# Kernel optimization log

Measured on AMD Instinct MI355X. Metric: run time of the kernel, lower is better.

## Reference

```python
import jax, jax.numpy as jnp
import numpy as np

N_NODES = 100000


def _gcn_conv(h, src, dst, norm, W, b):
    # h: [N, F_in] -> [N, F_out]; aggregate normalized messages over edges
    h = h @ W                                   # transform first (cheaper messages)
    msg = h[src] * norm[:, None]                # [E_tot, F_out]
    agg = jax.ops.segment_sum(msg, dst, num_segments=N_NODES)
    return agg + b


def setup_inputs() -> dict:
    key = jax.random.key(0)
    k1, k2, k3, k4 = jax.random.split(key, 4)
    x = jax.random.normal(k1, (N_NODES, 256), dtype=jnp.float32)
    edge_index = jax.random.randint(k2, (2, 1600000), 0, N_NODES, dtype=jnp.int64)
    W1 = jax.random.normal(k3, (256, 128), dtype=jnp.float32) * (1.0 / np.sqrt(256))
    b1 = jnp.zeros((128,), dtype=jnp.float32)
    W2 = jax.random.normal(k4, (128, 40), dtype=jnp.float32) * (1.0 / np.sqrt(128))
    b2 = jnp.zeros((40,), dtype=jnp.float32)
    return {"x": x, "edge_index": edge_index, "W1": W1, "b1": b1, "W2": W2, "b2": b2}


def reference(x, edge_index, W1, b1, W2, b2):
    # add self-loops
    loop = jnp.arange(N_NODES, dtype=edge_index.dtype)
    src = jnp.concatenate([edge_index[0], loop])
    dst = jnp.concatenate([edge_index[1], loop])
    # symmetric normalization D^{-1/2} (A+I) D^{-1/2}
    deg = jax.ops.segment_sum(jnp.ones_like(dst, dtype=x.dtype), dst, num_segments=N_NODES)
    dinv = jax.lax.rsqrt(jnp.maximum(deg, 1.0))
    norm = dinv[src] * dinv[dst]                # [E_tot]

    h = _gcn_conv(x, src, dst, norm, W1, b1)
    h = jax.nn.relu(h)                          # dropout p=0 / eval -> identity
    h = _gcn_conv(h, src, dst, norm, W2, b2)
    return jax.nn.log_softmax(h, axis=1)
```

## Files before the change

### kernel.cpp

```cpp
#include <hip/hip_runtime.h>
#include <hip/hip_fp8.h>
#include <math.h>

#define N_NODES 100000
#define N_EDGES 1600000
#define F_IN 256
#define F_H 128
#define F_OUT 40

#define BIN_SHIFT 9
#define BIN_NODES 512
#define NBIN 196
#define CAP 12288
#define CNT_PAD 16
#define PART_CHUNK 8192

typedef __attribute__((ext_vector_type(8))) short bf16x8;
typedef __attribute__((ext_vector_type(4))) float floatx4;
typedef __attribute__((ext_vector_type(2))) float floatx2;
typedef __attribute__((ext_vector_type(2))) unsigned int uintx2;

__device__ __forceinline__ unsigned short f2bf(float f) {
    unsigned int u = __float_as_uint(f);
    u += 0x7fffu + ((u >> 16) & 1u);
    return (unsigned short)(u >> 16);
}
__device__ __forceinline__ float bf2f(unsigned short s) { return __uint_as_float(((unsigned int)s) << 16); }

#if defined(__has_builtin)
#if __has_builtin(__builtin_amdgcn_cvt_pk_fp8_f32)
#define HAVE_PK_ENC 1
#endif
#if __has_builtin(__builtin_amdgcn_cvt_pk_f32_fp8)
#define HAVE_PK_DEC 1
#endif
#if __has_builtin(__builtin_amdgcn_cvt_f32_fp8)
#define HAVE_SC_DEC 1
#endif
#endif

__device__ __forceinline__ unsigned char f2f8(float f) {
#ifdef HAVE_PK_ENC
    int r = __builtin_amdgcn_cvt_pk_fp8_f32(f, f, 0, false);
    return (unsigned char)(r & 0xff);
#else
    __hip_fp8_e4m3 t(f);
    return (unsigned char)t.__x;
#endif
}
__device__ __forceinline__ float f82f(unsigned char b) {
#ifdef HAVE_SC_DEC
    return __builtin_amdgcn_cvt_f32_fp8((int)b, 0);
#else
    __hip_fp8_e4m3 t; t.__x = (__hip_fp8_storage_t)b;
    return (float)t;
#endif
}
__device__ __forceinline__ floatx2 f8x2tof(unsigned short u) {
#ifdef HAVE_PK_DEC
    return __builtin_amdgcn_cvt_pk_f32_fp8((int)u, false);
#else
    floatx2 r;
    r.x = f82f((unsigned char)(u & 0xff));
    r.y = f82f((unsigned char)(u >> 8));
    return r;
#endif
}

__global__ void k_zero(int* p, int n) {
    int i = blockIdx.x * blockDim.x + threadIdx.x;
    if (i < n) p[i] = 0;
}

__global__ __launch_bounds__(256) void k_part(const int* __restrict__ eidx,
                                              int* __restrict__ gcnt,
                                              unsigned int* __restrict__ parts) {
    __shared__ int hist[4][NBIN];
    __shared__ int sbase[NBIN];
    __shared__ int rcnt[NBIN];
    const int tid = threadIdx.x;
    const int wv = tid >> 6;
    for (int i = tid; i < NBIN; i += 256) {
        hist[0][i] = 0; hist[1][i] = 0; hist[2][i] = 0; hist[3][i] = 0; rcnt[i] = 0;
    }
    __syncthreads();
    const int e0 = blockIdx.x * PART_CHUNK;
    const int e1 = min(e0 + PART_CHUNK, N_EDGES);
    for (int e = e0 + tid; e < e1; e += 256) {
        int d = eidx[N_EDGES + e];
        atomicAdd(&hist[wv][d >> BIN_SHIFT], 1);
    }
    __syncthreads();
    for (int b = tid; b < NBIN; b += 256) {
        int tot = hist[0][b] + hist[1][b] + hist[2][b] + hist[3][b];
        int old = atomicAdd(&gcnt[b * CNT_PAD], tot);
        sbase[b] = b * CAP + old;
    }
    __syncthreads();
    for (int e = e0 + tid; e < e1; e += 256) {
        int d = eidx[N_EDGES + e];
        int s = eidx[e];
        int b = d >> BIN_SHIFT;
        int r = atomicAdd(&rcnt[b], 1);
        parts[sbase[b] + r] = ((unsigned int)s << BIN_SHIFT) | (unsigned int)(d & (BIN_NODES - 1));
    }
}

__global__ __launch_bounds__(256) void k_build(const unsigned int* __restrict__ parts,
                                               const int* __restrict__ gcnt,
                                               int* __restrict__ rowptr,
                                               float* __restrict__ dinv,
                                               int* __restrict__ csr_src) {
    __shared__ int deg[4][BIN_NODES];
    __shared__ int cur[BIN_NODES];
    __shared__ int scan[256];
    const int tid = threadIdx.x;
    const int wv = tid >> 6;
    const int g = blockIdx.x;

    scan[tid] = (tid < NBIN) ? gcnt[tid * CNT_PAD] : 0;
    __syncthreads();
    for (int off = 1; off < 256; off <<= 1) {
        int v = 0;
        if (tid >= off) v = scan[tid - off];
        __syncthreads();
        if (tid >= off) scan[tid] += v;
        __syncthreads();
    }
    const int binBase = (g == 0) ? 0 : scan[g - 1];
    const int cntg = scan[g] - binBase;

    for (int i = tid; i < BIN_NODES; i += 256) {
        deg[0][i] = 0; deg[1][i] = 0; deg[2][i] = 0; deg[3][i] = 0;
    }
    __syncthreads();

    const unsigned int* pp = parts + (size_t)g * CAP;
    for (int i = tid; i < cntg; i += 256)
        atomicAdd(&deg[wv][pp[i] & (BIN_NODES - 1)], 1);
    __syncthreads();

    const int n0 = 2 * tid, n1 = 2 * tid + 1;
    const int d0 = deg[0][n0] + deg[1][n0] + deg[2][n0] + deg[3][n0];
    const int d1 = deg[0][n1] + deg[1][n1] + deg[2][n1] + deg[3][n1];
    scan[tid] = d0 + d1;
    __syncthreads();
    for (int off = 1; off < 256; off <<= 1) {
        int v = 0;
        if (tid >= off) v = scan[tid - off];
        __syncthreads();
        if (tid >= off) scan[tid] += v;
        __syncthreads();
    }
    const int pre = (tid == 0) ? 0 : scan[tid - 1];
    const int p0 = binBase + pre;
    const int p1 = p0 + d0;
    const int node0 = g * BIN_NODES + n0;
    if (node0 < N_NODES)     { rowptr[node0]     = p0; dinv[node0]     = rsqrtf((float)d0 + 1.0f); }
    if (node0 + 1 < N_NODES) { rowptr[node0 + 1] = p1; dinv[node0 + 1] = rsqrtf((float)d1 + 1.0f); }
    cur[n0] = p0;
    cur[n1] = p1;
    __syncthreads();

    for (int i = tid; i < cntg; i += 256) {
        unsigned int u = pp[i];
        int pos = atomicAdd(&cur[u & (BIN_NODES - 1)], 1);
        csr_src[pos] = (int)(u >> BIN_SHIFT);
    }
    if (g == NBIN - 1 && tid == 0) rowptr[N_NODES] = N_EDGES;
}

__global__ void k_cvt_w(const float* __restrict__ W1, const float* __restrict__ W2,
                        short* __restrict__ W1t, short* __restrict__ W2t) {
    int b = blockIdx.x, t = threadIdx.x;
    if (b < 128) {
        int idx = b * 256 + t;
        int n = idx >> 8, k = idx & 255;
        W1t[n * 256 + k] = (short)f2bf(W1[k * 128 + n]);
    } else {
        int idx = (b - 128) * 256 + t;
        if (idx < 48 * 128) {
            int n = idx >> 7, k = idx & 127;
            float v = (n < F_OUT) ? W2[k * F_OUT + n] : 0.f;
            W2t[n * 128 + k] = (short)f2bf(v);
        }
    }
}

__global__ __launch_bounds__(256) void k_gemm1_mfma(const float* __restrict__ x,
                                                    const short* __restrict__ W1t,
                                                    const float* __restrict__ dinv,
                                                    unsigned char* __restrict__ h1f8) {
    __shared__ short As[64 * 40];
    __shared__ short Bs[128 * 40];
    __shared__ float Ds[64];
    const int tid = threadIdx.x;
    const int row0 = blockIdx.x * 64;
    const int w = tid >> 6, l = tid & 63;
    const int l15 = l & 15, q = l >> 4;
    const int ar = tid >> 2;
    const int ak = (tid & 3) * 8;
    const int bn = tid >> 1;
    const int bk = (tid & 1) * 16;

    if (tid < 64) {
        int r = row0 + tid;
        Ds[tid] = (r < N_NODES) ? dinv[r] : 0.f;
    }

    floatx4 acc[4][2];
#pragma unroll
    for (int mt = 0; mt < 4; ++mt)
#pragma unroll
        for (int nt = 0; nt < 2; ++nt) acc[mt][nt] = (floatx4)0.f;

    const bool arow_ok = (row0 + ar) < N_NODES;
    const float* xp = x + (size_t)(row0 + ar) * F_IN;

    for (int k0 = 0; k0 < F_IN; k0 += 32) {
        bf16x8 av;
        if (arow_ok) {
            float4 f0 = *(const float4*)(xp + k0 + ak);
            float4 f1 = *(const float4*)(xp + k0 + ak + 4);
            av[0] = (short)f2bf(f0.x); av[1] = (short)f2bf(f0.y);
            av[2] = (short)f2bf(f0.z); av[3] = (short)f2bf(f0.w);
            av[4] = (short)f2bf(f1.x); av[5] = (short)f2bf(f1.y);
            av[6] = (short)f2bf(f1.z); av[7] = (short)f2bf(f1.w);
        } else {
            av = (bf16x8)0;
        }
        *(bf16x8*)&As[ar * 40 + ak] = av;
        *(bf16x8*)&Bs[bn * 40 + bk]     = *(const bf16x8*)&W1t[bn * 256 + k0 + bk];
        *(bf16x8*)&Bs[bn * 40 + bk + 8] = *(const bf16x8*)&W1t[bn * 256 + k0 + bk + 8];
        __syncthreads();

        bf16x8 af[4], bfr[2];
#pragma unroll
        for (int mt = 0; mt < 4; ++mt)
            af[mt] = *(const bf16x8*)&As[(mt * 16 + l15) * 40 + q * 8];
#pragma unroll
        for (int nt = 0; nt < 2; ++nt)
            bfr[nt] = *(const bf16x8*)&Bs[(w * 32 + nt * 16 + l15) * 40 + q * 8];
#pragma unroll
        for (int mt = 0; mt < 4; ++mt)
#pragma unroll
            for (int nt = 0; nt < 2; ++nt)
                acc[mt][nt] = __builtin_amdgcn_mfma_f32_16x16x32_bf16(af[mt], bfr[nt], acc[mt][nt], 0, 0, 0);
        __syncthreads();
    }
#pragma unroll
    for (int mt = 0; mt < 4; ++mt) {
#pragma unroll
        for (int nt = 0; nt < 2; ++nt) {
            int col = w * 32 + nt * 16 + l15;
#pragma unroll
            for (int r = 0; r < 4; ++r) {
                int rl = mt * 16 + q * 4 + r;
                int row = row0 + rl;
                if (row < N_NODES)
                    h1f8[(size_t)row * F_H + col] = f2f8(acc[mt][nt][r] * Ds[rl]);
            }
        }
    }
}

__global__ __launch_bounds__(256) void k_spmm1(const int* __restrict__ rowptr,
                                               const int* __restrict__ csr_src,
                                               const unsigned int* __restrict__ h1d,
                                               const float* __restrict__ dinv,
                                               const float* __restrict__ b1,
                                               uintx2* __restrict__ agg1p2) {
    const int half = threadIdx.x >> 5;
    const int p = threadIdx.x & 31;
    int node = blockIdx.x * 8 + half;
    bool valid = node < N_NODES;
    int nd = valid ? node : 0;
    int beg = rowptr[nd];
    int end = valid ? rowptr[nd + 1] : beg;
    float dv = dinv[nd];

    unsigned int su = h1d[(size_t)nd * 32 + p];
    floatx2 s01 = f8x2tof((unsigned short)(su & 0xffffu));
    floatx2 s23 = f8x2tof((unsigned short)(su >> 16));
    float A0 = s01.x, A1 = s01.y, A2 = s23.x, A3 = s23.y;
    float B0 = 0.f, B1 = 0.f, B2 = 0.f, B3 = 0.f;
    float C0 = 0.f, C1 = 0.f, C2 = 0.f, C3 = 0.f;
    float D0 = 0.f, D1 = 0.f, D2 = 0.f, D3 = 0.f;

    int i = beg;
    for (; i + 3 < end; i += 4) {
        int s0 = csr_src[i], s1 = csr_src[i + 1], s2 = csr_src[i + 2], s3 = csr_src[i + 3];
        unsigned int u0 = h1d[(size_t)s0 * 32 + p];
        unsigned int u1 = h1d[(size_t)s1 * 32 + p];
        unsigned int u2 = h1d[(size_t)s2 * 32 + p];
        unsigned int u3 = h1d[(size_t)s3 * 32 + p];
        floatx2 a01 = f8x2tof((unsigned short)(u0 & 0xffffu));
        floatx2 a23 = f8x2tof((unsigned short)(u0 >> 16));
        floatx2 b01 = f8x2tof((unsigned short)(u1 & 0xffffu));
        floatx2 b23 = f8x2tof((unsigned short)(u1 >> 16));
        floatx2 c01 = f8x2tof((unsigned short)(u2 & 0xffffu));
        floatx2 c23 = f8x2tof((unsigned short)(u2 >> 16));
        floatx2 d01 = f8x2tof((unsigned short)(u3 & 0xffffu));
        floatx2 d23 = f8x2tof((unsigned short)(u3 >> 16));
        A0 += a01.x; A1 += a01.y; A2 += a23.x; A3 += a23.y;
        B0 += b01.x; B1 += b01.y; B2 += b23.x; B3 += b23.y;
        C0 += c01.x; C1 += c01.y; C2 += c23.x; C3 += c23.y;
        D0 += d01.x; D1 += d01.y; D2 += d23.x; D3 += d23.y;
    }
    for (; i < end; ++i) {
        unsigned int u0 = h1d[(size_t)csr_src[i] * 32 + p];
        floatx2 a01 = f8x2tof((unsigned short)(u0 & 0xffffu));
        floatx2 a23 = f8x2tof((unsigned short)(u0 >> 16));
        A0 += a01.x; A1 += a01.y; A2 += a23.x; A3 += a23.y;
    }

    float4 bb = *(const float4*)&b1[4 * p];
    float v0 = fmaf((A0 + B0) + (C0 + D0), dv, bb.x);
    float v1 = fmaf((A1 + B1) + (C1 + D1), dv, bb.y);
    float v2 = fmaf((A2 + B2) + (C2 + D2), dv, bb.z);
    float v3 = fmaf((A3 + B3) + (C3 + D3), dv, bb.w);
    v0 = v0 > 0.f ? v0 : 0.f;
    v1 = v1 > 0.f ? v1 : 0.f;
    v2 = v2 > 0.f ? v2 : 0.f;
    v3 = v3 > 0.f ? v3 : 0.f;
    if (valid) {
        uintx2 o;
        o.x = ((unsigned int)f2bf(v1) << 16) | f2bf(v0);
        o.y = ((unsigned int)f2bf(v3) << 16) | f2bf(v2);
        agg1p2[(size_t)node * 32 + p] = o;
    }
}

__global__ __launch_bounds__(256) void k_gemm2_mfma(const unsigned short* __restrict__ agg1b,
                                                    const short* __restrict__ W2t,
                                                    const float* __restrict__ dinv,
                                                    unsigned char* __restrict__ h2f8) {
    __shared__ short As[128 * 40];
    __shared__ short Bs[48 * 136];
    __shared__ float Ds[128];
    const int tid = threadIdx.x;
    const int row0 = blockIdx.x * 128;
    const int w = tid >> 6, l = tid & 63;
    const int l15 = l & 15, q = l >> 4;
    const int ar = tid >> 1;
    const int ak = (tid & 1) * 16;

#pragma unroll
    for (int i = 0; i < 3; ++i) {
        int c = tid * 3 + i;
        int n = c >> 4, koff = (c & 15) * 8;
        *(bf16x8*)&Bs[n * 136 + koff] = *(const bf16x8*)&W2t[n * 128 + koff];
    }
    if (tid < 128) {
        int r = row0 + tid;
        Ds[tid] = (r < N_NODES) ? dinv[r] : 0.f;
    }

    floatx4 acc[2][3];
#pragma unroll
    for (int a = 0; a < 2; ++a)
#pragma unroll
        for (int nt = 0; nt < 3; ++nt) acc[a][nt] = (floatx4)0.f;

    const bool arow_ok = (row0 + ar) < N_NODES;
    const unsigned short* ap = agg1b + (size_t)(row0 + ar) * F_H;

    for (int k0 = 0; k0 < F_H; k0 += 32) {
        bf16x8 a0, a1;
        if (arow_ok) {
            a0 = *(const bf16x8*)(ap + k0 + ak);
            a1 = *(const bf16x8*)(ap + k0 + ak + 8);
        } else {
            a0 = (bf16x8)0; a1 = (bf16x8)0;
        }
        *(bf16x8*)&As[ar * 40 + ak]     = a0;
        *(bf16x8*)&As[ar * 40 + ak + 8] = a1;
        __syncthreads();

        bf16x8 af[2], bfr[3];
#pragma unroll
        for (int a = 0; a < 2; ++a)
            af[a] = *(const bf16x8*)&As[((w * 2 + a) * 16 + l15) * 40 + q * 8];
#pragma unroll
        for (int nt = 0; nt < 3; ++nt)
            bfr[nt] = *(const bf16x8*)&Bs[(nt * 16 + l15) * 136 + k0 + q * 8];
#pragma unroll
        for (int a = 0; a < 2; ++a)
#pragma unroll
            for (int nt = 0; nt < 3; ++nt)
                acc[a][nt] = __builtin_amdgcn_mfma_f32_16x16x32_bf16(af[a], bfr[nt], acc[a][nt], 0, 0, 0);
        __syncthreads();
    }
#pragma unroll
    for (int a = 0; a < 2; ++a) {
#pragma unroll
        for (int nt = 0; nt < 3; ++nt) {
            int col = nt * 16 + l15;
#pragma unroll
            for (int r = 0; r < 4; ++r) {
                int rl = (w * 2 + a) * 16 + q * 4 + r;
                int row = row0 + rl;
                if (row < N_NODES && col < F_OUT)
                    h2f8[(size_t)row * F_OUT + col] = f2f8(acc[a][nt][r] * Ds[rl]);
            }
        }
    }
}

__global__ __launch_bounds__(256) void k_spmm2_lsm(const int* __restrict__ rowptr,
                                                   const int* __restrict__ csr_src,
                                                   const unsigned int* __restrict__ h2d,
                                                   const float* __restrict__ dinv,
                                                   const float* __restrict__ b2,
                                                   float* __restrict__ out) {
    const int qid = threadIdx.x >> 4;
    const int p = threadIdx.x & 15;
    int node = blockIdx.x * 16 + qid;
    bool nvalid = node < N_NODES;
    bool valid = nvalid && (p < 10);
    int nd = nvalid ? node : 0;
    int beg = 0, end = 0;
    if (valid) { beg = rowptr[nd]; end = rowptr[nd + 1]; }
    float dv = dinv[nd];

    float A0 = 0.f, A1 = 0.f, A2 = 0.f, A3 = 0.f;
    float B0 = 0.f, B1 = 0.f, B2 = 0.f, B3 = 0.f;
    if (valid) {
        unsigned int su = h2d[(size_t)nd * 10 + p];
        floatx2 t0 = f8x2tof((unsigned short)(su & 0xffffu));
        floatx2 t1 = f8x2tof((unsigned short)(su >> 16));
        A0 = t0.x; A1 = t0.y; A2 = t1.x; A3 = t1.y;
    }
    int i = beg;
    for (; i + 1 < end; i += 2) {
        int s0 = csr_src[i], s1 = csr_src[i + 1];
        unsigned int u0 = h2d[(size_t)s0 * 10 + p];
        unsigned int u1 = h2d[(size_t)s1 * 10 + p];
        floatx2 a01 = f8x2tof((unsigned short)(u0 & 0xffffu));
        floatx2 a23 = f8x2tof((unsigned short)(u0 >> 16));
        floatx2 b01 = f8x2tof((unsigned short)(u1 & 0xffffu));
        floatx2 b23 = f8x2tof((unsigned short)(u1 >> 16));
        A0 += a01.x; A1 += a01.y; A2 += a23.x; A3 += a23.y;
        B0 += b01.x; B1 += b01.y; B2 += b23.x; B3 += b23.y;
    }
    if (i < end) {
        unsigned int u0 = h2d[(size_t)csr_src[i] * 10 + p];
        floatx2 a01 = f8x2tof((unsigned short)(u0 & 0xffffu));
        floatx2 a23 = f8x2tof((unsigned short)(u0 >> 16));
        A0 += a01.x; A1 += a01.y; A2 += a23.x; A3 += a23.y;
    }

    float v0 = -INFINITY, v1 = -INFINITY, v2 = -INFINITY, v3 = -INFINITY;
    if (valid) {
        float4 bb = *(const float4*)&b2[4 * p];
        v0 = fmaf(A0 + B0, dv, bb.x);
        v1 = fmaf(A1 + B1, dv, bb.y);
        v2 = fmaf(A2 + B2, dv, bb.z);
        v3 = fmaf(A3 + B3, dv, bb.w);
    }
    float m = fmaxf(fmaxf(v0, v1), fmaxf(v2, v3));
#pragma unroll
    for (int off = 1; off < 16; off <<= 1) m = fmaxf(m, __shfl_xor(m, off, 16));
    float e = 0.f;
    if (valid) e = expf(v0 - m) + expf(v1 - m) + expf(v2 - m) + expf(v3 - m);
#pragma unroll
    for (int off = 1; off < 16; off <<= 1) e += __shfl_xor(e, off, 16);
    if (valid) {
        float ls = logf(e);
        float4 o;
        o.x = v0 - m - ls; o.y = v1 - m - ls; o.z = v2 - m - ls; o.w = v3 - m - ls;
        *(float4*)&out[(size_t)node * F_OUT + 4 * p] = o;
    }
}

extern "C" void kernel_launch(void* const* d_in, const int* in_sizes, int n_in,
                              void* d_out, int out_size, void* d_ws, size_t ws_size,
                              hipStream_t stream) {
    const float* x = (const float*)d_in[0];
    const int* eidx = (const int*)d_in[1];
    const float* W1 = (const float*)d_in[2];
    const float* b1 = (const float*)d_in[3];
    const float* W2 = (const float*)d_in[4];
    const float* b2 = (const float*)d_in[5];
    float* out = (float*)d_out;

    char* ws = (char*)d_ws;
    int*   gcnt      = (int*)  (ws);
    int*   rowptr    = (int*)  (ws + 400512);
    int*   csr_src   = (int*)  (ws + 1200528);
    float* dinv      = (float*)(ws + 7600528);
    short* W1t       = (short*)(ws + 8000528);
    short* W2t       = (short*)(ws + 8066064);
    unsigned char*  h1f8  = (unsigned char*) (ws + 8078352);
    unsigned short* agg1b = (unsigned short*)(ws + 20878352);
    unsigned int*   parts = (unsigned int*)  (ws + 20878352);
    unsigned char*  h2f8  = (unsigned char*) (ws + 46478352);

    k_zero<<<(NBIN * CNT_PAD + 255) / 256, 256, 0, stream>>>(gcnt, NBIN * CNT_PAD);
    k_part<<<(N_EDGES + PART_CHUNK - 1) / PART_CHUNK, 256, 0, stream>>>(eidx, gcnt, parts);
    k_build<<<NBIN, 256, 0, stream>>>(parts, gcnt, rowptr, dinv, csr_src);

    k_cvt_w<<<152, 256, 0, stream>>>(W1, W2, W1t, W2t);

    k_gemm1_mfma<<<(N_NODES + 63) / 64, 256, 0, stream>>>(x, W1t, dinv, h1f8);
    k_spmm1<<<(N_NODES + 7) / 8, 256, 0, stream>>>(rowptr, csr_src,
                                                   (const unsigned int*)h1f8, dinv, b1,
                                                   (uintx2*)agg1b);
    k_gemm2_mfma<<<(N_NODES + 127) / 128, 256, 0, stream>>>(agg1b, W2t, dinv, h2f8);
    k_spmm2_lsm<<<(N_NODES + 15) / 16, 256, 0, stream>>>(rowptr, csr_src,
                                                         (const unsigned int*)h2f8, dinv, b2, out);
}
```

Baseline: 340.3 us.

## Split hidden features into four column planes for cache-friendly SpMM gathers

GEMM1 now keeps W1 fragments in registers with no LDS staging, and writes h1 as four 32-column fp8 planes instead of one row-major 128-column array. SpMM1 runs once per plane, so the random gathers for each pass hit a 3.2 MB table that fits in cache better, at the cost of reading the CSR indices four times and launching four kernels. Nontemporal loads and stores are added for streamed x, csr indices and outputs to reduce cache pollution.

```diff
diff --git a/kernel.cpp b/kernel.cpp
--- a/kernel.cpp
+++ b/kernel.cpp
@@ -190,96 +190,70 @@
 __global__ __launch_bounds__(256) void k_gemm1_mfma(const float* __restrict__ x,
                                                     const short* __restrict__ W1t,
                                                     const float* __restrict__ dinv,
-                                                    unsigned char* __restrict__ h1f8) {
-    __shared__ short As[64 * 40];
-    __shared__ short Bs[128 * 40];
-    __shared__ float Ds[64];
+                                                    unsigned char* __restrict__ h1q) {
     const int tid = threadIdx.x;
-    const int row0 = blockIdx.x * 64;
     const int w = tid >> 6, l = tid & 63;
     const int l15 = l & 15, q = l >> 4;
-    const int ar = tid >> 2;
-    const int ak = (tid & 3) * 8;
-    const int bn = tid >> 1;
-    const int bk = (tid & 1) * 16;
-
-    if (tid < 64) {
-        int r = row0 + tid;
-        Ds[tid] = (r < N_NODES) ? dinv[r] : 0.f;
-    }
-
-    floatx4 acc[4][2];
-#pragma unroll
-    for (int mt = 0; mt < 4; ++mt)
-#pragma unroll
-        for (int nt = 0; nt < 2; ++nt) acc[mt][nt] = (floatx4)0.f;
-
-    const bool arow_ok = (row0 + ar) < N_NODES;
-    const float* xp = x + (size_t)(row0 + ar) * F_IN;
-
-    for (int k0 = 0; k0 < F_IN; k0 += 32) {
-        bf16x8 av;
-        if (arow_ok) {
-            float4 f0 = *(const float4*)(xp + k0 + ak);
-            float4 f1 = *(const float4*)(xp + k0 + ak + 4);
-            av[0] = (short)f2bf(f0.x); av[1] = (short)f2bf(f0.y);
-            av[2] = (short)f2bf(f0.z); av[3] = (short)f2bf(f0.w);
-            av[4] = (short)f2bf(f1.x); av[5] = (short)f2bf(f1.y);
-            av[6] = (short)f2bf(f1.z); av[7] = (short)f2bf(f1.w);
-        } else {
-            av = (bf16x8)0;
+    const int row0 = blockIdx.x * 128;
+
+    bf16x8 breg[2][8];
+#pragma unroll
+    for (int nt = 0; nt < 2; ++nt)
+#pragma unroll
+        for (int ks = 0; ks < 8; ++ks)
+            breg[nt][ks] = *(const bf16x8*)&W1t[(w * 32 + nt * 16 + l15) * 256 + ks * 32 + q * 8];
+
+    unsigned char* const hbase = h1q + (size_t)w * N_NODES * 32;
+
+#pragma unroll 1
+    for (int mt = 0; mt < 8; ++mt) {
+        const int arow = row0 + mt * 16 + l15;
+        const bool ok = arow < N_NODES;
+        const float* xp = x + (size_t)arow * F_IN + q * 8;
+        floatx4 acc0 = (floatx4)0.f, acc1 = (floatx4)0.f;
+#pragma unroll
+        for (int ks = 0; ks < 8; ++ks) {
+            bf16x8 af = (bf16x8)0;
+            if (ok) {
+                floatx4 f0 = __builtin_nontemporal_load((const floatx4*)(xp + ks * 32));
+                floatx4 f1 = __builtin_nontemporal_load((const floatx4*)(xp + ks * 32 + 4));
+                af[0] = (short)f2bf(f0[0]); af[1] = (short)f2bf(f0[1]);
+                af[2] = (short)f2bf(f0[2]); af[3] = (short)f2bf(f0[3]);
+                af[4] = (short)f2bf(f1[0]); af[5] = (short)f2bf(f1[1]);
+                af[6] = (short)f2bf(f1[2]); af[7] = (short)f2bf(f1[3]);
+            }
+            acc0 = __builtin_amdgcn_mfma_f32_16x16x32_bf16(af, breg[0][ks], acc0, 0, 0, 0);
+            acc1 = __builtin_amdgcn_mfma_f32_16x16x32_bf16(af, breg[1][ks], acc1, 0, 0, 0);
         }
-        *(bf16x8*)&As[ar * 40 + ak] = av;
-        *(bf16x8*)&Bs[bn * 40 + bk]     = *(const bf16x8*)&W1t[bn * 256 + k0 + bk];
-        *(bf16x8*)&Bs[bn * 40 + bk + 8] = *(const bf16x8*)&W1t[bn * 256 + k0 + bk + 8];
-        __syncthreads();
-
-        bf16x8 af[4], bfr[2];
-#pragma unroll
-        for (int mt = 0; mt < 4; ++mt)
-            af[mt] = *(const bf16x8*)&As[(mt * 16 + l15) * 40 + q * 8];
-#pragma unroll
-        for (int nt = 0; nt < 2; ++nt)
-            bfr[nt] = *(const bf16x8*)&Bs[(w * 32 + nt * 16 + l15) * 40 + q * 8];
-#pragma unroll
-        for (int mt = 0; mt < 4; ++mt)
-#pragma unroll
-            for (int nt = 0; nt < 2; ++nt)
-                acc[mt][nt] = __builtin_amdgcn_mfma_f32_16x16x32_bf16(af[mt], bfr[nt], acc[mt][nt], 0, 0, 0);
-        __syncthreads();
-    }
-#pragma unroll
-    for (int mt = 0; mt < 4; ++mt) {
-#pragma unroll
-        for (int nt = 0; nt < 2; ++nt) {
-            int col = w * 32 + nt * 16 + l15;
-#pragma unroll
-            for (int r = 0; r < 4; ++r) {
-                int rl = mt * 16 + q * 4 + r;
-                int row = row0 + rl;
-                if (row < N_NODES)
-                    h1f8[(size_t)row * F_H + col] = f2f8(acc[mt][nt][r] * Ds[rl]);
+#pragma unroll
+        for (int r = 0; r < 4; ++r) {
+            const int row = row0 + mt * 16 + q * 4 + r;
+            if (row < N_NODES) {
+                const float ds = dinv[row];
+                unsigned char* hp = hbase + (size_t)row * 32;
+                hp[l15]      = f2f8(acc0[r] * ds);
+                hp[16 + l15] = f2f8(acc1[r] * ds);
             }
         }
     }
 }
 
-__global__ __launch_bounds__(256) void k_spmm1(const int* __restrict__ rowptr,
-                                               const int* __restrict__ csr_src,
-                                               const unsigned int* __restrict__ h1d,
-                                               const float* __restrict__ dinv,
-                                               const float* __restrict__ b1,
-                                               uintx2* __restrict__ agg1p2) {
-    const int half = threadIdx.x >> 5;
-    const int p = threadIdx.x & 31;
-    int node = blockIdx.x * 8 + half;
+__global__ __launch_bounds__(256) void k_spmm1_q(const int* __restrict__ rowptr,
+                                                 const int* __restrict__ csr_src,
+                                                 const unsigned int* __restrict__ hq,
+                                                 const float* __restrict__ dinv,
+                                                 const float* __restrict__ b1p,
+                                                 unsigned short* __restrict__ aggp) {
+    const int oct = threadIdx.x >> 3;
+    const int p = threadIdx.x & 7;
+    int node = blockIdx.x * 32 + oct;
     bool valid = node < N_NODES;
     int nd = valid ? node : 0;
     int beg = rowptr[nd];
     int end = valid ? rowptr[nd + 1] : beg;
     float dv = dinv[nd];
 
-    unsigned int su = h1d[(size_t)nd * 32 + p];
+    unsigned int su = hq[(size_t)nd * 8 + p];
     floatx2 s01 = f8x2tof((unsigned short)(su & 0xffffu));
     floatx2 s23 = f8x2tof((unsigned short)(su >> 16));
     float A0 = s01.x, A1 = s01.y, A2 = s23.x, A3 = s23.y;
@@ -289,11 +263,14 @@
 
     int i = beg;
     for (; i + 3 < end; i += 4) {
-        int s0 = csr_src[i], s1 = csr_src[i + 1], s2 = csr_src[i + 2], s3 = csr_src[i + 3];
-        unsigned int u0 = h1d[(size_t)s0 * 32 + p];
-        unsigned int u1 = h1d[(size_t)s1 * 32 + p];
-        unsigned int u2 = h1d[(size_t)s2 * 32 + p];
-        unsigned int u3 = h1d[(size_t)s3 * 32 + p];
+        int s0 = __builtin_nontemporal_load(csr_src + i);
+        int s1 = __builtin_nontemporal_load(csr_src + i + 1);
+        int s2 = __builtin_nontemporal_load(csr_src + i + 2);
+        int s3 = __builtin_nontemporal_load(csr_src + i + 3);
+        unsigned int u0 = hq[(size_t)s0 * 8 + p];
+        unsigned int u1 = hq[(size_t)s1 * 8 + p];
+        unsigned int u2 = hq[(size_t)s2 * 8 + p];
+        unsigned int u3 = hq[(size_t)s3 * 8 + p];
         floatx2 a01 = f8x2tof((unsigned short)(u0 & 0xffffu));
         floatx2 a23 = f8x2tof((unsigned short)(u0 >> 16));
         floatx2 b01 = f8x2tof((unsigned short)(u1 & 0xffffu));
@@ -308,13 +285,14 @@
         D0 += d01.x; D1 += d01.y; D2 += d23.x; D3 += d23.y;
     }
     for (; i < end; ++i) {
-        unsigned int u0 = h1d[(size_t)csr_src[i] * 32 + p];
+        int s0 = __builtin_nontemporal_load(csr_src + i);
+        unsigned int u0 = hq[(size_t)s0 * 8 + p];
         floatx2 a01 = f8x2tof((unsigned short)(u0 & 0xffffu));
         floatx2 a23 = f8x2tof((unsigned short)(u0 >> 16));
         A0 += a01.x; A1 += a01.y; A2 += a23.x; A3 += a23.y;
     }
 
-    float4 bb = *(const float4*)&b1[4 * p];
+    float4 bb = *(const float4*)&b1p[4 * p];
     float v0 = fmaf((A0 + B0) + (C0 + D0), dv, bb.x);
     float v1 = fmaf((A1 + B1) + (C1 + D1), dv, bb.y);
     float v2 = fmaf((A2 + B2) + (C2 + D2), dv, bb.z);
@@ -327,7 +305,7 @@
         uintx2 o;
         o.x = ((unsigned int)f2bf(v1) << 16) | f2bf(v0);
         o.y = ((unsigned int)f2bf(v3) << 16) | f2bf(v2);
-        agg1p2[(size_t)node * 32 + p] = o;
+        __builtin_nontemporal_store(o, (uintx2*)&aggp[(size_t)node * F_H + 4 * p]);
     }
 }
 
@@ -433,7 +411,8 @@
     }
     int i = beg;
     for (; i + 1 < end; i += 2) {
-        int s0 = csr_src[i], s1 = csr_src[i + 1];
+        int s0 = __builtin_nontemporal_load(csr_src + i);
+        int s1 = __builtin_nontemporal_load(csr_src + i + 1);
         unsigned int u0 = h2d[(size_t)s0 * 10 + p];
         unsigned int u1 = h2d[(size_t)s1 * 10 + p];
         floatx2 a01 = f8x2tof((unsigned short)(u0 & 0xffffu));
@@ -444,7 +423,8 @@
         B0 += b01.x; B1 += b01.y; B2 += b23.x; B3 += b23.y;
     }
     if (i < end) {
-        unsigned int u0 = h2d[(size_t)csr_src[i] * 10 + p];
+        int s0 = __builtin_nontemporal_load(csr_src + i);
+        unsigned int u0 = h2d[(size_t)s0 * 10 + p];
         floatx2 a01 = f8x2tof((unsigned short)(u0 & 0xffffu));
         floatx2 a23 = f8x2tof((unsigned short)(u0 >> 16));
         A0 += a01.x; A1 += a01.y; A2 += a23.x; A3 += a23.y;
@@ -467,9 +447,9 @@
     for (int off = 1; off < 16; off <<= 1) e += __shfl_xor(e, off, 16);
     if (valid) {
         float ls = logf(e);
-        float4 o;
-        o.x = v0 - m - ls; o.y = v1 - m - ls; o.z = v2 - m - ls; o.w = v3 - m - ls;
-        *(float4*)&out[(size_t)node * F_OUT + 4 * p] = o;
+        floatx4 o;
+        o[0] = v0 - m - ls; o[1] = v1 - m - ls; o[2] = v2 - m - ls; o[3] = v3 - m - ls;
+        __builtin_nontemporal_store(o, (floatx4*)&out[(size_t)node * F_OUT + 4 * p]);
     }
 }
 
@@ -491,7 +471,7 @@
     float* dinv      = (float*)(ws + 7600528);
     short* W1t       = (short*)(ws + 8000528);
     short* W2t       = (short*)(ws + 8066064);
-    unsigned char*  h1f8  = (unsigned char*) (ws + 8078352);
+    unsigned char*  h1q   = (unsigned char*) (ws + 8078352);
     unsigned short* agg1b = (unsigned short*)(ws + 20878352);
     unsigned int*   parts = (unsigned int*)  (ws + 20878352);
     unsigned char*  h2f8  = (unsigned char*) (ws + 46478352);
@@ -502,10 +482,14 @@
 
     k_cvt_w<<<152, 256, 0, stream>>>(W1, W2, W1t, W2t);
 
-    k_gemm1_mfma<<<(N_NODES + 63) / 64, 256, 0, stream>>>(x, W1t, dinv, h1f8);
-    k_spmm1<<<(N_NODES + 7) / 8, 256, 0, stream>>>(rowptr, csr_src,
-                                                   (const unsigned int*)h1f8, dinv, b1,
-                                                   (uintx2*)agg1b);
+    k_gemm1_mfma<<<(N_NODES + 127) / 128, 256, 0, stream>>>(x, W1t, dinv, h1q);
+
+    for (int pl = 0; pl < 4; ++pl)
+        k_spmm1_q<<<(N_NODES + 31) / 32, 256, 0, stream>>>(
+            rowptr, csr_src,
+            (const unsigned int*)h1q + (size_t)pl * N_NODES * 8,
+            dinv, b1 + pl * 32, agg1b + pl * 32);
+
     k_gemm2_mfma<<<(N_NODES + 127) / 128, 256, 0, stream>>>(agg1b, W2t, dinv, h2f8);
     k_spmm2_lsm<<<(N_NODES + 15) / 16, 256, 0, stream>>>(rowptr, csr_src,
                                                          (const unsigned int*)h2f8, dinv, b2, out);
```

After: 454.6 us. 1.34x slower.

## Rewrite gemm1 to register-resident W1 fragments with double-buffered x loads

Applied to the files above, without the earlier changes.

The first-layer GEMM kernel drops its shared-memory staging and barriers. Each wave keeps its full W1 bf16 fragment set in registers and loads x rows straight from global memory into MFMA operand layout, double-buffering two 16-row tiles so loads overlap compute. The output log-softmax store becomes a nontemporal store. The cost is heavy register use (16 bf16x8 B fragments plus 32 floatx4 A buffers), which may lower occupancy. Each lane's x reads are also less coalesced, since it fetches 32-byte segments at 128-byte strides.

```diff
diff --git a/kernel.cpp b/kernel.cpp
--- a/kernel.cpp
+++ b/kernel.cpp
@@ -187,81 +187,69 @@
     }
 }
 
+__device__ __forceinline__ void g1_load(const float* __restrict__ x, int row0, int mt,
+                                        int l15, int q, floatx4 f0[8], floatx4 f1[8]) {
+    const int arow = row0 + mt * 16 + l15;
+    const bool ok = arow < N_NODES;
+    const float* xp = x + (size_t)arow * F_IN + q * 8;
+#pragma unroll
+    for (int ks = 0; ks < 8; ++ks) {
+        f0[ks] = ok ? *(const floatx4*)(xp + ks * 32) : (floatx4)0.f;
+        f1[ks] = ok ? *(const floatx4*)(xp + ks * 32 + 4) : (floatx4)0.f;
+    }
+}
+__device__ __forceinline__ void g1_comp(const floatx4 f0[8], const floatx4 f1[8],
+                                        const bf16x8* breg,
+                                        const float* __restrict__ dinv,
+                                        unsigned char* __restrict__ h1f8,
+                                        int row0, int mt, int w, int l15, int q) {
+    floatx4 acc0 = (floatx4)0.f, acc1 = (floatx4)0.f;
+#pragma unroll
+    for (int ks = 0; ks < 8; ++ks) {
+        bf16x8 af;
+        af[0] = (short)f2bf(f0[ks][0]); af[1] = (short)f2bf(f0[ks][1]);
+        af[2] = (short)f2bf(f0[ks][2]); af[3] = (short)f2bf(f0[ks][3]);
+        af[4] = (short)f2bf(f1[ks][0]); af[5] = (short)f2bf(f1[ks][1]);
+        af[6] = (short)f2bf(f1[ks][2]); af[7] = (short)f2bf(f1[ks][3]);
+        acc0 = __builtin_amdgcn_mfma_f32_16x16x32_bf16(af, breg[ks], acc0, 0, 0, 0);
+        acc1 = __builtin_amdgcn_mfma_f32_16x16x32_bf16(af, breg[8 + ks], acc1, 0, 0, 0);
+    }
+#pragma unroll
+    for (int r = 0; r < 4; ++r) {
+        const int row = row0 + mt * 16 + q * 4 + r;
+        if (row < N_NODES) {
+            const float ds = dinv[row];
+            unsigned char* hp = h1f8 + (size_t)row * F_H + w * 32;
+            hp[l15]      = f2f8(acc0[r] * ds);
+            hp[16 + l15] = f2f8(acc1[r] * ds);
+        }
+    }
+}
 __global__ __launch_bounds__(256) void k_gemm1_mfma(const float* __restrict__ x,
                                                     const short* __restrict__ W1t,
                                                     const float* __restrict__ dinv,
                                                     unsigned char* __restrict__ h1f8) {
-    __shared__ short As[64 * 40];
-    __shared__ short Bs[128 * 40];
-    __shared__ float Ds[64];
     const int tid = threadIdx.x;
-    const int row0 = blockIdx.x * 64;
     const int w = tid >> 6, l = tid & 63;
     const int l15 = l & 15, q = l >> 4;
-    const int ar = tid >> 2;
-    const int ak = (tid & 3) * 8;
-    const int bn = tid >> 1;
-    const int bk = (tid & 1) * 16;
-
-    if (tid < 64) {
-        int r = row0 + tid;
-        Ds[tid] = (r < N_NODES) ? dinv[r] : 0.f;
-    }
-
-    floatx4 acc[4][2];
-#pragma unroll
-    for (int mt = 0; mt < 4; ++mt)
-#pragma unroll
-        for (int nt = 0; nt < 2; ++nt) acc[mt][nt] = (floatx4)0.f;
-
-    const bool arow_ok = (row0 + ar) < N_NODES;
-    const float* xp = x + (size_t)(row0 + ar) * F_IN;
-
-    for (int k0 = 0; k0 < F_IN; k0 += 32) {
-        bf16x8 av;
-        if (arow_ok) {
-            float4 f0 = *(const float4*)(xp + k0 + ak);
-            float4 f1 = *(const float4*)(xp + k0 + ak + 4);
-            av[0] = (short)f2bf(f0.x); av[1] = (short)f2bf(f0.y);
-            av[2] = (short)f2bf(f0.z); av[3] = (short)f2bf(f0.w);
-            av[4] = (short)f2bf(f1.x); av[5] = (short)f2bf(f1.y);
-            av[6] = (short)f2bf(f1.z); av[7] = (short)f2bf(f1.w);
-        } else {
-            av = (bf16x8)0;
-        }
-        *(bf16x8*)&As[ar * 40 + ak] = av;
-        *(bf16x8*)&Bs[bn * 40 + bk]     = *(const bf16x8*)&W1t[bn * 256 + k0 + bk];
-        *(bf16x8*)&Bs[bn * 40 + bk + 8] = *(const bf16x8*)&W1t[bn * 256 + k0 + bk + 8];
-        __syncthreads();
-
-        bf16x8 af[4], bfr[2];
-#pragma unroll
-        for (int mt = 0; mt < 4; ++mt)
-            af[mt] = *(const bf16x8*)&As[(mt * 16 + l15) * 40 + q * 8];
-#pragma unroll
-        for (int nt = 0; nt < 2; ++nt)
-            bfr[nt] = *(const bf16x8*)&Bs[(w * 32 + nt * 16 + l15) * 40 + q * 8];
-#pragma unroll
-        for (int mt = 0; mt < 4; ++mt)
-#pragma unroll
-            for (int nt = 0; nt < 2; ++nt)
-                acc[mt][nt] = __builtin_amdgcn_mfma_f32_16x16x32_bf16(af[mt], bfr[nt], acc[mt][nt], 0, 0, 0);
-        __syncthreads();
-    }
-#pragma unroll
-    for (int mt = 0; mt < 4; ++mt) {
-#pragma unroll
-        for (int nt = 0; nt < 2; ++nt) {
-            int col = w * 32 + nt * 16 + l15;
-#pragma unroll
-            for (int r = 0; r < 4; ++r) {
-                int rl = mt * 16 + q * 4 + r;
-                int row = row0 + rl;
-                if (row < N_NODES)
-                    h1f8[(size_t)row * F_H + col] = f2f8(acc[mt][nt][r] * Ds[rl]);
-            }
-        }
-    }
+    const int row0 = blockIdx.x * 64;
+
+    bf16x8 breg[16];
+#pragma unroll
+    for (int nt = 0; nt < 2; ++nt)
+#pragma unroll
+        for (int ks = 0; ks < 8; ++ks)
+            breg[nt * 8 + ks] = *(const bf16x8*)&W1t[(w * 32 + nt * 16 + l15) * 256 + ks * 32 + q * 8];
+
+    floatx4 aA0[8], aA1[8], aB0[8], aB1[8];
+    g1_load(x, row0, 0, l15, q, aA0, aA1);
+    g1_load(x, row0, 1, l15, q, aB0, aB1);
+    g1_comp(aA0, aA1, breg, dinv, h1f8, row0, 0, w, l15, q);
+    g1_load(x, row0, 2, l15, q, aA0, aA1);
+    g1_comp(aB0, aB1, breg, dinv, h1f8, row0, 1, w, l15, q);
+    g1_load(x, row0, 3, l15, q, aB0, aB1);
+    g1_comp(aA0, aA1, breg, dinv, h1f8, row0, 2, w, l15, q);
+    g1_comp(aB0, aB1, breg, dinv, h1f8, row0, 3, w, l15, q);
 }
 
 __global__ __launch_bounds__(256) void k_spmm1(const int* __restrict__ rowptr,
@@ -467,9 +455,9 @@
     for (int off = 1; off < 16; off <<= 1) e += __shfl_xor(e, off, 16);
     if (valid) {
         float ls = logf(e);
-        float4 o;
-        o.x = v0 - m - ls; o.y = v1 - m - ls; o.z = v2 - m - ls; o.w = v3 - m - ls;
-        *(float4*)&out[(size_t)node * F_OUT + 4 * p] = o;
+        floatx4 o;
+        o[0] = v0 - m - ls; o[1] = v1 - m - ls; o[2] = v2 - m - ls; o[3] = v3 - m - ls;
+        __builtin_nontemporal_store(o, (floatx4*)&out[(size_t)node * F_OUT + 4 * p]);
     }
 }
 
```

Measured after the change: 450.1 us. 1.32x slower.

## Preload full W1 into LDS and enlarge GEMM1 row tile to 128

Applied to the files above, without the earlier changes.

GEMM1 now keeps the whole transposed bf16 W1 (128x256, padded) resident in shared memory, loaded once per block. The row tile grows from 64 to 128, with each wave owning 32 rows across all 128 columns. This removes the per-k-step reload of B from global memory and halves the number of blocks. The cost is about 75KB of LDS per block, which lowers occupancy and limits overlap of the x loads. Separately, the final log-softmax output is written with nontemporal stores.

```diff
diff --git a/kernel.cpp b/kernel.cpp
--- a/kernel.cpp
+++ b/kernel.cpp
@@ -191,74 +191,83 @@
                                                     const short* __restrict__ W1t,
                                                     const float* __restrict__ dinv,
                                                     unsigned char* __restrict__ h1f8) {
-    __shared__ short As[64 * 40];
-    __shared__ short Bs[128 * 40];
-    __shared__ float Ds[64];
+    __shared__ short As[128 * 40];
+    __shared__ short Bs[128 * 264];
+    __shared__ float Ds[128];
     const int tid = threadIdx.x;
-    const int row0 = blockIdx.x * 64;
+    const int row0 = blockIdx.x * 128;
     const int w = tid >> 6, l = tid & 63;
     const int l15 = l & 15, q = l >> 4;
-    const int ar = tid >> 2;
-    const int ak = (tid & 3) * 8;
-    const int bn = tid >> 1;
-    const int bk = (tid & 1) * 16;
-
-    if (tid < 64) {
+    const int ar = tid >> 1;
+    const int ak = (tid & 1) * 16;
+
+    {
+        const int n = tid >> 1;
+        const int kh = (tid & 1) * 128;
+#pragma unroll
+        for (int i = 0; i < 16; ++i)
+            *(bf16x8*)&Bs[n * 264 + kh + i * 8] = *(const bf16x8*)&W1t[n * 256 + kh + i * 8];
+    }
+    if (tid < 128) {
         int r = row0 + tid;
         Ds[tid] = (r < N_NODES) ? dinv[r] : 0.f;
     }
 
-    floatx4 acc[4][2];
-#pragma unroll
-    for (int mt = 0; mt < 4; ++mt)
-#pragma unroll
-        for (int nt = 0; nt < 2; ++nt) acc[mt][nt] = (floatx4)0.f;
+    floatx4 acc[2][8];
+#pragma unroll
+    for (int a = 0; a < 2; ++a)
+#pragma unroll
+        for (int nt = 0; nt < 8; ++nt) acc[a][nt] = (floatx4)0.f;
 
     const bool arow_ok = (row0 + ar) < N_NODES;
     const float* xp = x + (size_t)(row0 + ar) * F_IN;
 
     for (int k0 = 0; k0 < F_IN; k0 += 32) {
-        bf16x8 av;
+        bf16x8 av0 = (bf16x8)0, av1 = (bf16x8)0;
         if (arow_ok) {
-            float4 f0 = *(const float4*)(xp + k0 + ak);
-            float4 f1 = *(const float4*)(xp + k0 + ak + 4);
-            av[0] = (short)f2bf(f0.x); av[1] = (short)f2bf(f0.y);
-            av[2] = (short)f2bf(f0.z); av[3] = (short)f2bf(f0.w);
-            av[4] = (short)f2bf(f1.x); av[5] = (short)f2bf(f1.y);
-            av[6] = (short)f2bf(f1.z); av[7] = (short)f2bf(f1.w);
-        } else {
-            av = (bf16x8)0;
+            floatx4 f0 = *(const floatx4*)(xp + k0 + ak);
+            floatx4 f1 = *(const floatx4*)(xp + k0 + ak + 4);
+            floatx4 f2 = *(const floatx4*)(xp + k0 + ak + 8);
+            floatx4 f3 = *(const floatx4*)(xp + k0 + ak + 12);
+            av0[0] = (short)f2bf(f0[0]); av0[1] = (short)f2bf(f0[1]);
+            av0[2] = (short)f2bf(f0[2]); av0[3] = (short)f2bf(f0[3]);
+            av0[4] = (short)f2bf(f1[0]); av0[5] = (short)f2bf(f1[1]);
+            av0[6] = (short)f2bf(f1[2]); av0[7] = (short)f2bf(f1[3]);
+            av1[0] = (short)f2bf(f2[0]); av1[1] = (short)f2bf(f2[1]);
+            av1[2] = (short)f2bf(f2[2]); av1[3] = (short)f2bf(f2[3]);
+            av1[4] = (short)f2bf(f3[0]); av1[5] = (short)f2bf(f3[1]);
+            av1[6] = (short)f2bf(f3[2]); av1[7] = (short)f2bf(f3[3]);
         }
-        *(bf16x8*)&As[ar * 40 + ak] = av;
-        *(bf16x8*)&Bs[bn * 40 + bk]     = *(const bf16x8*)&W1t[bn * 256 + k0 + bk];
-        *(bf16x8*)&Bs[bn * 40 + bk + 8] = *(const bf16x8*)&W1t[bn * 256 + k0 + bk + 8];
-        __syncthreads();
-
-        bf16x8 af[4], bfr[2];
-#pragma unroll
-        for (int mt = 0; mt < 4; ++mt)
-            af[mt] = *(const bf16x8*)&As[(mt * 16 + l15) * 40 + q * 8];
-#pragma unroll
-        for (int nt = 0; nt < 2; ++nt)
-            bfr[nt] = *(const bf16x8*)&Bs[(w * 32 + nt * 16 + l15) * 40 + q * 8];
-#pragma unroll
-        for (int mt = 0; mt < 4; ++mt)
-#pragma unroll
-            for (int nt = 0; nt < 2; ++nt)
-                acc[mt][nt] = __builtin_amdgcn_mfma_f32_16x16x32_bf16(af[mt], bfr[nt], acc[mt][nt], 0, 0, 0);
-        __syncthreads();
-    }
-#pragma unroll
-    for (int mt = 0; mt < 4; ++mt) {
-#pragma unroll
-        for (int nt = 0; nt < 2; ++nt) {
-            int col = w * 32 + nt * 16 + l15;
-#pragma unroll
-            for (int r = 0; r < 4; ++r) {
-                int rl = mt * 16 + q * 4 + r;
-                int row = row0 + rl;
-                if (row < N_NODES)
-                    h1f8[(size_t)row * F_H + col] = f2f8(acc[mt][nt][r] * Ds[rl]);
+        __syncthreads();
+        *(bf16x8*)&As[ar * 40 + ak]     = av0;
+        *(bf16x8*)&As[ar * 40 + ak + 8] = av1;
+        __syncthreads();
+
+        bf16x8 af[2], bfr[8];
+#pragma unroll
+        for (int a = 0; a < 2; ++a)
+            af[a] = *(const bf16x8*)&As[((w * 2 + a) * 16 + l15) * 40 + q * 8];
+#pragma unroll
+        for (int nt = 0; nt < 8; ++nt)
+            bfr[nt] = *(const bf16x8*)&Bs[(nt * 16 + l15) * 264 + k0 + q * 8];
+#pragma unroll
+        for (int a = 0; a < 2; ++a)
+#pragma unroll
+            for (int nt = 0; nt < 8; ++nt)
+                acc[a][nt] = __builtin_amdgcn_mfma_f32_16x16x32_bf16(af[a], bfr[nt], acc[a][nt], 0, 0, 0);
+    }
+#pragma unroll
+    for (int a = 0; a < 2; ++a) {
+#pragma unroll
+        for (int r = 0; r < 4; ++r) {
+            const int rl = (w * 2 + a) * 16 + q * 4 + r;
+            const int row = row0 + rl;
+            if (row < N_NODES) {
+                const float ds = Ds[rl];
+                unsigned char* hp = h1f8 + (size_t)row * F_H;
+#pragma unroll
+                for (int nt = 0; nt < 8; ++nt)
+                    hp[nt * 16 + l15] = f2f8(acc[a][nt][r] * ds);
             }
         }
     }
@@ -467,9 +476,9 @@
     for (int off = 1; off < 16; off <<= 1) e += __shfl_xor(e, off, 16);
     if (valid) {
         float ls = logf(e);
-        float4 o;
-        o.x = v0 - m - ls; o.y = v1 - m - ls; o.z = v2 - m - ls; o.w = v3 - m - ls;
-        *(float4*)&out[(size_t)node * F_OUT + 4 * p] = o;
+        floatx4 o;
+        o[0] = v0 - m - ls; o[1] = v1 - m - ls; o[2] = v2 - m - ls; o[3] = v3 - m - ls;
+        __builtin_nontemporal_store(o, (floatx4*)&out[(size_t)node * F_OUT + 4 * p]);
     }
 }
 
@@ -502,7 +511,7 @@
 
     k_cvt_w<<<152, 256, 0, stream>>>(W1, W2, W1t, W2t);
 
-    k_gemm1_mfma<<<(N_NODES + 63) / 64, 256, 0, stream>>>(x, W1t, dinv, h1f8);
+    k_gemm1_mfma<<<(N_NODES + 127) / 128, 256, 0, stream>>>(x, W1t, dinv, h1f8);
     k_spmm1<<<(N_NODES + 7) / 8, 256, 0, stream>>>(rowptr, csr_src,
                                                    (const unsigned int*)h1f8, dinv, b1,
                                                    (uintx2*)agg1b);
```

Result: no change. 339.7 us (-0.2%).
